# Performance work log

Hardware: AMD Instinct MI355X
Metric: run time of the kernel (lower is better)

Reference implementation:

```python
import jax, jax.numpy as jnp
import numpy as np

EPS = 1e-10
B = 524288

def setup_inputs() -> dict:
    key = jax.random.key(0)
    k1, k2, k3, k4, k5 = jax.random.split(key, 5)
    return {
        "out1": jax.random.normal(k1, (B, 8), dtype=jnp.float32),
        "out2": jax.random.normal(k2, (B, 6), dtype=jnp.float32),
        "out3": jax.random.normal(k3, (B, 6), dtype=jnp.float32),
        "out4": jax.random.normal(k4, (B, 9), dtype=jnp.float32),
        "label": jax.random.uniform(k5, (B, 29), dtype=jnp.float32),
    }

def _head_loss(logits, lbl):
    # per-sample softmax over tiny vocab, then weighted NLL with eps inside log
    p = jax.nn.softmax(logits, axis=-1)
    return -jnp.sum(jnp.log(p + EPS) * lbl)

def reference(out1, out2, out3, out4, label):
    l1 = _head_loss(out1, label[:, 0:8])
    l2 = _head_loss(out2, label[:, 8:14])
    l3 = _head_loss(out3, label[:, 14:20])
    l4 = _head_loss(out4, label[:, 20:29])
    n = out1.shape[0]
    return (l1 + l2 + l3 + l4) / n
```

## Files before the change

kernel.cpp:

```cpp
#include <hip/hip_runtime.h>
#include <cmath>

#define NROWS 524288
#define NBLOCKS (NROWS / 256)
#define EPS 1e-10f

template <int N>
__device__ __forceinline__ float head_loss(const float* x, const float* lbl) {
    float m = -INFINITY;
    #pragma unroll
    for (int i = 0; i < N; ++i) m = fmaxf(m, x[i]);
    float e[N];
    float s = 0.f;
    #pragma unroll
    for (int i = 0; i < N; ++i) { e[i] = __expf(x[i] - m); s += e[i]; }
    float inv = 1.0f / s;
    float acc = 0.f;
    #pragma unroll
    for (int i = 0; i < N; ++i) acc += __logf(e[i] * inv + EPS) * lbl[i];
    return -acc;
}

__global__ __launch_bounds__(256, 5) void fused_loss_kernel(
    const float* __restrict__ o1, const float* __restrict__ o2,
    const float* __restrict__ o3, const float* __restrict__ o4,
    const float* __restrict__ lbl, double* __restrict__ partial) {
    __shared__ float slbl[256 * 29];
    __shared__ double sacc[4];

    const int tid = threadIdx.x;
    const int wid = tid >> 6;
    const int lane = tid & 63;
    const size_t blk = blockIdx.x;

    {
        const float4* src = reinterpret_cast<const float4*>(lbl + blk * (256 * 29)) + wid * 464;
        float4* dst = reinterpret_cast<float4*>(slbl) + wid * 464;
        #pragma unroll
        for (int k = 0; k < 7; ++k) dst[lane + 64 * k] = src[lane + 64 * k];
        if (lane < 16) dst[lane + 448] = src[lane + 448];
    }

    const size_t i = blk * 256 + tid;

    float v1[8];
    {
        const float4* p = reinterpret_cast<const float4*>(o1 + i * 8);
        float4 a = p[0], b = p[1];
        v1[0] = a.x; v1[1] = a.y; v1[2] = a.z; v1[3] = a.w;
        v1[4] = b.x; v1[5] = b.y; v1[6] = b.z; v1[7] = b.w;
    }
    float v2[6], v3[6];
    {
        const float2* p = reinterpret_cast<const float2*>(o2 + i * 6);
        float2 a = p[0], b = p[1], c = p[2];
        v2[0] = a.x; v2[1] = a.y; v2[2] = b.x; v2[3] = b.y; v2[4] = c.x; v2[5] = c.y;
    }
    {
        const float2* p = reinterpret_cast<const float2*>(o3 + i * 6);
        float2 a = p[0], b = p[1], c = p[2];
        v3[0] = a.x; v3[1] = a.y; v3[2] = b.x; v3[3] = b.y; v3[4] = c.x; v3[5] = c.y;
    }
    float v4[9];
    {
        const float* p = o4 + i * 9;
        #pragma unroll
        for (int j = 0; j < 9; ++j) v4[j] = p[j];
    }

    const float* lrow = slbl + tid * 29;

    float loss;
    loss  = head_loss<8>(v1, lrow + 0);
    loss += head_loss<6>(v2, lrow + 8);
    loss += head_loss<6>(v3, lrow + 14);
    loss += head_loss<9>(v4, lrow + 20);

    double d = (double)loss;
    #pragma unroll
    for (int off = 32; off > 0; off >>= 1) d += __shfl_down(d, off);

    if (lane == 0) sacc[wid] = d;
    __syncthreads();
    if (tid == 0) partial[blk] = sacc[0] + sacc[1] + sacc[2] + sacc[3];
}

__global__ __launch_bounds__(256) void reduce_kernel(const double* __restrict__ partial,
                                                     float* __restrict__ out) {
    double s = 0.0;
    for (int i = threadIdx.x; i < NBLOCKS; i += 256) s += partial[i];
    #pragma unroll
    for (int off = 32; off > 0; off >>= 1) s += __shfl_down(s, off);
    __shared__ double sa[4];
    const int wid = threadIdx.x >> 6;
    if ((threadIdx.x & 63) == 0) sa[wid] = s;
    __syncthreads();
    if (threadIdx.x == 0) out[0] = (float)((sa[0] + sa[1] + sa[2] + sa[3]) / (double)NROWS);
}

extern "C" void kernel_launch(void* const* d_in, const int* in_sizes, int n_in,
                              void* d_out, int out_size, void* d_ws, size_t ws_size,
                              hipStream_t stream) {
    const float* o1  = (const float*)d_in[0];
    const float* o2  = (const float*)d_in[1];
    const float* o3  = (const float*)d_in[2];
    const float* o4  = (const float*)d_in[3];
    const float* lbl = (const float*)d_in[4];
    double* partial = (double*)d_ws;

    fused_loss_kernel<<<NBLOCKS, 256, 0, stream>>>(o1, o2, o3, o4, lbl, partial);
    reduce_kernel<<<1, 256, 0, stream>>>(partial, (float*)d_out);
}
```

Before: 28.67 us.

## Stage labels and odd-width logits into LDS via direct global-to-LDS loads

Replaces the register-path label copy and the per-thread strided loads of out2, out3 and out4 with `global_load_lds` 16-byte transfers, so each wave loads its own 64 rows straight into shared memory. Each thread then reads its row from LDS, behind a `vmcnt(0)` wait and a schedule barrier. The intent is to turn the narrow strided loads of the 6- and 9-wide rows into fully coalesced wide loads and skip the VGPR round-trip for the label tile. In exchange, per-block LDS grows to about 50 KB and the min-blocks launch hint is dropped, which may lower occupancy for this memory-bound kernel.

Result: slower. 31.88 us (+11.2%).

```diff
diff --git a/kernel.cpp b/kernel.cpp
--- a/kernel.cpp
+++ b/kernel.cpp
@@ -4,6 +4,14 @@
 #define NROWS 524288
 #define NBLOCKS (NROWS / 256)
 #define EPS 1e-10f
+
+typedef float f4 __attribute__((ext_vector_type(4)));
+
+__device__ __forceinline__ void glds16(const float* gp, float* lp) {
+    __builtin_amdgcn_global_load_lds(
+        (const __attribute__((address_space(1))) void*)(gp),
+        (__attribute__((address_space(3))) void*)(lp), 16, 0, 0);
+}
 
 template <int N>
 __device__ __forceinline__ float head_loss(const float* x, const float* lbl) {
@@ -21,11 +29,14 @@
     return -acc;
 }
 
-__global__ __launch_bounds__(256, 5) void fused_loss_kernel(
+__global__ __launch_bounds__(256) void fused_loss_kernel(
     const float* __restrict__ o1, const float* __restrict__ o2,
     const float* __restrict__ o3, const float* __restrict__ o4,
     const float* __restrict__ lbl, double* __restrict__ partial) {
     __shared__ float slbl[256 * 29];
+    __shared__ float so4[256 * 9];
+    __shared__ float so2[256 * 6];
+    __shared__ float so3[256 * 6];
     __shared__ double sacc[4];
 
     const int tid = threadIdx.x;
@@ -33,48 +44,57 @@
     const int lane = tid & 63;
     const size_t blk = blockIdx.x;
 
-    {
-        const float4* src = reinterpret_cast<const float4*>(lbl + blk * (256 * 29)) + wid * 464;
-        float4* dst = reinterpret_cast<float4*>(slbl) + wid * 464;
-        #pragma unroll
-        for (int k = 0; k < 7; ++k) dst[lane + 64 * k] = src[lane + 64 * k];
-        if (lane < 16) dst[lane + 448] = src[lane + 448];
+    const float* gl  = lbl + (blk * 1856 + (size_t)wid * 464) * 4;
+    const float* g4  = o4  + (blk * 576  + (size_t)wid * 144) * 4;
+    const float* g2  = o2  + (blk * 384  + (size_t)wid * 96)  * 4;
+    const float* g3  = o3  + (blk * 384  + (size_t)wid * 96)  * 4;
+    float* ll = slbl + (size_t)wid * 464 * 4;
+    float* l4 = so4  + (size_t)wid * 144 * 4;
+    float* l2 = so2  + (size_t)wid * 96 * 4;
+    float* l3 = so3  + (size_t)wid * 96 * 4;
+
+    #pragma unroll
+    for (int k = 0; k < 7; ++k) glds16(gl + (lane + 64 * k) * 4, ll + k * 256);
+    #pragma unroll
+    for (int k = 0; k < 2; ++k) glds16(g4 + (lane + 64 * k) * 4, l4 + k * 256);
+    glds16(g2 + lane * 4, l2);
+    glds16(g3 + lane * 4, l3);
+
+    if (lane < 16) {
+        f4 t = reinterpret_cast<const f4*>(gl)[448 + lane];
+        reinterpret_cast<f4*>(ll)[448 + lane] = t;
+        f4 u = reinterpret_cast<const f4*>(g4)[128 + lane];
+        reinterpret_cast<f4*>(l4)[128 + lane] = u;
+    }
+    if (lane < 32) {
+        f4 t = reinterpret_cast<const f4*>(g2)[64 + lane];
+        reinterpret_cast<f4*>(l2)[64 + lane] = t;
+        f4 u = reinterpret_cast<const f4*>(g3)[64 + lane];
+        reinterpret_cast<f4*>(l3)[64 + lane] = u;
     }
 
     const size_t i = blk * 256 + tid;
-
     float v1[8];
     {
-        const float4* p = reinterpret_cast<const float4*>(o1 + i * 8);
-        float4 a = p[0], b = p[1];
+        const f4* p = reinterpret_cast<const f4*>(o1 + i * 8);
+        f4 a = p[0], b = p[1];
         v1[0] = a.x; v1[1] = a.y; v1[2] = a.z; v1[3] = a.w;
         v1[4] = b.x; v1[5] = b.y; v1[6] = b.z; v1[7] = b.w;
     }
-    float v2[6], v3[6];
-    {
-        const float2* p = reinterpret_cast<const float2*>(o2 + i * 6);
-        float2 a = p[0], b = p[1], c = p[2];
-        v2[0] = a.x; v2[1] = a.y; v2[2] = b.x; v2[3] = b.y; v2[4] = c.x; v2[5] = c.y;
-    }
-    {
-        const float2* p = reinterpret_cast<const float2*>(o3 + i * 6);
-        float2 a = p[0], b = p[1], c = p[2];
-        v3[0] = a.x; v3[1] = a.y; v3[2] = b.x; v3[3] = b.y; v3[4] = c.x; v3[5] = c.y;
-    }
-    float v4[9];
-    {
-        const float* p = o4 + i * 9;
-        #pragma unroll
-        for (int j = 0; j < 9; ++j) v4[j] = p[j];
-    }
+
+    asm volatile("s_waitcnt vmcnt(0)" ::: "memory");
+    __builtin_amdgcn_sched_barrier(0);
 
     const float* lrow = slbl + tid * 29;
+    const float* r4   = so4 + tid * 9;
+    const float* r2   = so2 + tid * 6;
+    const float* r3   = so3 + tid * 6;
 
     float loss;
     loss  = head_loss<8>(v1, lrow + 0);
-    loss += head_loss<6>(v2, lrow + 8);
-    loss += head_loss<6>(v3, lrow + 14);
-    loss += head_loss<9>(v4, lrow + 20);
+    loss += head_loss<6>(r2, lrow + 8);
+    loss += head_loss<6>(r3, lrow + 14);
+    loss += head_loss<9>(r4, lrow + 20);
 
     double d = (double)loss;
     #pragma unroll
```

## Replace second reduction kernel with atomic last-block finalize and vectorize o4 loads

Applied to the files above, without the earlier changes.

Removes the separate single-block reduce kernel. Each block now atomically adds its double partial sum into a global accumulator, and the last block to arrive, tracked by an atomic counter, writes the final mean. A memset of the workspace is added to reset the accumulator and counter on every call. The o4 row loads are also changed to two unaligned float4 vector loads plus one scalar load, replacing nine scalar loads. Contention on a single double atomic and the extra memset launch are the costs, and the summation order is no longer deterministic.

Result: slower. 87.72 us (+206.0%).

```diff
diff --git a/kernel.cpp b/kernel.cpp
--- a/kernel.cpp
+++ b/kernel.cpp
@@ -4,6 +4,9 @@
 #define NROWS 524288
 #define NBLOCKS (NROWS / 256)
 #define EPS 1e-10f
+
+typedef float f4 __attribute__((ext_vector_type(4)));
+typedef float f4u __attribute__((ext_vector_type(4), aligned(4)));
 
 template <int N>
 __device__ __forceinline__ float head_loss(const float* x, const float* lbl) {
@@ -24,7 +27,8 @@
 __global__ __launch_bounds__(256, 5) void fused_loss_kernel(
     const float* __restrict__ o1, const float* __restrict__ o2,
     const float* __restrict__ o3, const float* __restrict__ o4,
-    const float* __restrict__ lbl, double* __restrict__ partial) {
+    const float* __restrict__ lbl, double* __restrict__ gsum,
+    unsigned* __restrict__ gcnt, float* __restrict__ out) {
     __shared__ float slbl[256 * 29];
     __shared__ double sacc[4];
 
@@ -34,8 +38,8 @@
     const size_t blk = blockIdx.x;
 
     {
-        const float4* src = reinterpret_cast<const float4*>(lbl + blk * (256 * 29)) + wid * 464;
-        float4* dst = reinterpret_cast<float4*>(slbl) + wid * 464;
+        const f4* src = reinterpret_cast<const f4*>(lbl + blk * (256 * 29)) + wid * 464;
+        f4* dst = reinterpret_cast<f4*>(slbl) + wid * 464;
         #pragma unroll
         for (int k = 0; k < 7; ++k) dst[lane + 64 * k] = src[lane + 64 * k];
         if (lane < 16) dst[lane + 448] = src[lane + 448];
@@ -45,8 +49,8 @@
 
     float v1[8];
     {
-        const float4* p = reinterpret_cast<const float4*>(o1 + i * 8);
-        float4 a = p[0], b = p[1];
+        const f4* p = reinterpret_cast<const f4*>(o1 + i * 8);
+        f4 a = p[0], b = p[1];
         v1[0] = a.x; v1[1] = a.y; v1[2] = a.z; v1[3] = a.w;
         v1[4] = b.x; v1[5] = b.y; v1[6] = b.z; v1[7] = b.w;
     }
@@ -63,9 +67,11 @@
     }
     float v4[9];
     {
-        const float* p = o4 + i * 9;
-        #pragma unroll
-        for (int j = 0; j < 9; ++j) v4[j] = p[j];
+        const f4u* p = reinterpret_cast<const f4u*>(o4 + i * 9);
+        f4u a = p[0], b = p[1];
+        v4[0] = a.x; v4[1] = a.y; v4[2] = a.z; v4[3] = a.w;
+        v4[4] = b.x; v4[5] = b.y; v4[6] = b.z; v4[7] = b.w;
+        v4[8] = o4[i * 9 + 8];
     }
 
     const float* lrow = slbl + tid * 29;
@@ -82,20 +88,17 @@
 
     if (lane == 0) sacc[wid] = d;
     __syncthreads();
-    if (tid == 0) partial[blk] = sacc[0] + sacc[1] + sacc[2] + sacc[3];
-}
-
-__global__ __launch_bounds__(256) void reduce_kernel(const double* __restrict__ partial,
-                                                     float* __restrict__ out) {
-    double s = 0.0;
-    for (int i = threadIdx.x; i < NBLOCKS; i += 256) s += partial[i];
-    #pragma unroll
-    for (int off = 32; off > 0; off >>= 1) s += __shfl_down(s, off);
-    __shared__ double sa[4];
-    const int wid = threadIdx.x >> 6;
-    if ((threadIdx.x & 63) == 0) sa[wid] = s;
-    __syncthreads();
-    if (threadIdx.x == 0) out[0] = (float)((sa[0] + sa[1] + sa[2] + sa[3]) / (double)NROWS);
+    if (tid == 0) {
+        double part = sacc[0] + sacc[1] + sacc[2] + sacc[3];
+        atomicAdd(gsum, part);
+        __threadfence();
+        unsigned old = atomicAdd(gcnt, 1u);
+        if (old == NBLOCKS - 1) {
+            __threadfence();
+            double s = atomicAdd(gsum, 0.0);
+            out[0] = (float)(s / (double)NROWS);
+        }
+    }
 }
 
 extern "C" void kernel_launch(void* const* d_in, const int* in_sizes, int n_in,
@@ -106,8 +109,10 @@
     const float* o3  = (const float*)d_in[2];
     const float* o4  = (const float*)d_in[3];
     const float* lbl = (const float*)d_in[4];
-    double* partial = (double*)d_ws;
+    double* gsum = (double*)d_ws;
+    unsigned* gcnt = (unsigned*)((char*)d_ws + 8);
 
-    fused_loss_kernel<<<NBLOCKS, 256, 0, stream>>>(o1, o2, o3, o4, lbl, partial);
-    reduce_kernel<<<1, 256, 0, stream>>>(partial, (float*)d_out);
+    hipMemsetAsync(d_ws, 0, 16, stream);
+    fused_loss_kernel<<<NBLOCKS, 256, 0, stream>>>(o1, o2, o3, o4, lbl,
+                                                   gsum, gcnt, (float*)d_out);
 }
```
